# Optimization experiments

Hardware: AMD Instinct MI355X
Metric: run time of the kernel (lower is better)

The kernel has to match this reference:

```python
import jax, jax.numpy as jnp
import numpy as np

N, E, D = 50000, 800000, 128
BN_EPS = 1e-5
COORDS_WEIGHT = 1.0


def _p(key, shape, scale=0.05):
    return (jax.random.normal(key, shape, dtype=jnp.float32) * scale)


def setup_inputs() -> dict:
    key = jax.random.key(0)
    ks = jax.random.split(key, 16)
    inp = {
        "h": jax.random.normal(ks[0], (N, D), dtype=jnp.float32),
        "coord": jax.random.normal(ks[1], (N, 3), dtype=jnp.float32),
        "edge_index": jax.random.randint(ks[2], (2, E), 0, N, dtype=jnp.int32),
        # edge_mlp: Linear(2D+1 -> D), BN, ReLU, Linear(D -> D), BN, ReLU
        "e_w1": _p(ks[3], (D, 2 * D + 1)), "e_b1": jnp.zeros((D,), jnp.float32),
        "e_g1": jnp.ones((D,), jnp.float32), "e_be1": jnp.zeros((D,), jnp.float32),
        "e_w2": _p(ks[4], (D, D)), "e_b2": jnp.zeros((D,), jnp.float32),
        "e_g2": jnp.ones((D,), jnp.float32), "e_be2": jnp.zeros((D,), jnp.float32),
        # node_mlp: Linear(D + D -> D), BN, ReLU, Linear(D -> D)
        "n_w1": _p(ks[5], (D, 2 * D)), "n_b1": jnp.zeros((D,), jnp.float32),
        "n_g1": jnp.ones((D,), jnp.float32), "n_be1": jnp.zeros((D,), jnp.float32),
        "n_w2": _p(ks[6], (D, D)), "n_b2": jnp.zeros((D,), jnp.float32),
        # coord_mlp: Linear(D -> D), BN, ReLU, Linear(D -> 1, bias=False, tiny init)
        "c_w1": _p(ks[7], (D, D)), "c_b1": jnp.zeros((D,), jnp.float32),
        "c_g1": jnp.ones((D,), jnp.float32), "c_be1": jnp.zeros((D,), jnp.float32),
        "c_w2": _p(ks[8], (1, D), scale=0.001),
    }
    return inp


def _bn(x, g, b):
    # BatchNorm1d in training mode: biased batch stats over dim 0
    m = jnp.mean(x, axis=0)
    v = jnp.var(x, axis=0)
    return (x - m) * jax.lax.rsqrt(v + BN_EPS) * g + b


def _segment_mean(data, seg, num_segments):
    s = jax.ops.segment_sum(data, seg, num_segments=num_segments)
    c = jax.ops.segment_sum(jnp.ones((data.shape[0], 1), data.dtype), seg,
                            num_segments=num_segments)
    return s / jnp.maximum(c, 1.0)


def reference(h, coord, edge_index,
              e_w1, e_b1, e_g1, e_be1, e_w2, e_b2, e_g2, e_be2,
              n_w1, n_b1, n_g1, n_be1, n_w2, n_b2,
              c_w1, c_b1, c_g1, c_be1, c_w2):
    row, col = edge_index[0], edge_index[1]
    # coord2radial
    coord_diff = coord[row] - coord[col]                      # [E,3]
    radial = jnp.sum(coord_diff ** 2, axis=1, keepdims=True)  # [E,1]
    # edge_model
    e_in = jnp.concatenate([h[row], h[col], radial], axis=1)  # [E, 2D+1]
    x = jax.nn.relu(_bn(e_in @ e_w1.T + e_b1, e_g1, e_be1))
    edge_feat = jax.nn.relu(_bn(x @ e_w2.T + e_b2, e_g2, e_be2))  # [E,D]
    # coord_model
    y = jax.nn.relu(_bn(edge_feat @ c_w1.T + c_b1, c_g1, c_be1))
    scale = y @ c_w2.T                                        # [E,1]
    trans = jnp.clip(coord_diff * scale, -100.0, 100.0)
    coord_out = coord + _segment_mean(trans, row, coord.shape[0]) * COORDS_WEIGHT
    # node_model
    agg = _segment_mean(edge_feat, row, h.shape[0])           # [N,D]
    n_in = jnp.concatenate([h, agg], axis=1)                  # [N,2D]
    z = jax.nn.relu(_bn(n_in @ n_w1.T + n_b1, n_g1, n_be1))
    h_out = h + (z @ n_w2.T + n_b2)                           # recurrent residual
    return (h_out, coord_out)
```

## Files before the change

### kernel.cpp

```cpp
#include <hip/hip_runtime.h>

#define Nn 50000
#define En 800000
#define NSLOT 64

typedef __attribute__((ext_vector_type(8))) short short8;
typedef __attribute__((ext_vector_type(4))) float f32x4;

union U8 { uint4 u4; unsigned short us[8]; short8 s8; };

static __device__ __forceinline__ float bf2f(unsigned int lo16) {
  return __uint_as_float(lo16 << 16);
}
static __device__ __forceinline__ unsigned short f2bf(float f) {
  unsigned int x = __float_as_uint(f);
  return (unsigned short)((x + 0x7FFFu + ((x >> 16) & 1u)) >> 16);
}


__global__ __launch_bounds__(256) void k_prep_h(const float* __restrict__ h,
                                                unsigned short* __restrict__ nodeA) {
  int idx = blockIdx.x * 256 + threadIdx.x;
  if (idx >= Nn * 128) return;
  int n = idx >> 7, k = idx & 127;
  nodeA[(size_t)n * 256 + k] = f2bf(h[idx]);
}

__global__ __launch_bounds__(256) void k_prep_w(const float* __restrict__ src,
                                                unsigned short* __restrict__ dst, int Ksrc,
                                                int koff, int kshift, int total) {
  int idx = blockIdx.x * 256 + threadIdx.x;
  if (idx >= total) return;
  int n = idx >> kshift;
  int k = idx & ((1 << kshift) - 1);
  dst[idx] = f2bf(src[n * Ksrc + koff + k]);
}

__global__ void k_wlast(const float* __restrict__ e_w1, float* __restrict__ wlast) {
  int t = threadIdx.x;
  if (t < 128) wlast[t] = e_w1[t * 257 + 256];
}


__global__ __launch_bounds__(256) void k_count(const int* __restrict__ row, int* __restrict__ cnt) {
  int e = blockIdx.x * 256 + threadIdx.x;
  atomicAdd(&cnt[row[e]], 1);
}

__global__ __launch_bounds__(256) void k_fill(const int* __restrict__ row,
                                              const int* __restrict__ col,
                                              int* __restrict__ cursor,
                                              unsigned short* __restrict__ rowS,
                                              unsigned short* __restrict__ colS) {
  int e = blockIdx.x * 256 + threadIdx.x;
  int r = row[e];
  int pos = atomicAdd(&cursor[r], 1);
  rowS[pos] = (unsigned short)r;
  colS[pos] = (unsigned short)col[e];
}

__global__ __launch_bounds__(1024) void k_scan(const int* __restrict__ cnt, int* __restrict__ start,
                                               int* __restrict__ cursor, int n) {
  __shared__ int wsum[16];
  __shared__ int carry;
  int tid = threadIdx.x, lane = tid & 63, wid = tid >> 6;
  if (tid == 0) carry = 0;
  __syncthreads();
  for (int base = 0; base < n; base += 1024) {
    int i = base + tid;
    int v = (i < n) ? cnt[i] : 0;
    int x = v;
#pragma unroll
    for (int d = 1; d < 64; d <<= 1) {
      int y = __shfl_up(x, d, 64);
      if (lane >= d) x += y;
    }
    if (lane == 63) wsum[wid] = x;
    __syncthreads();
    if (wid == 0) {
      int s = (lane < 16) ? wsum[lane] : 0;
#pragma unroll
      for (int d = 1; d < 16; d <<= 1) {
        int y = __shfl_up(s, d, 64);
        if (lane >= d) s += y;
      }
      if (lane < 16) wsum[lane] = s;
    }
    __syncthreads();
    int c0 = carry;
    int waveoff = (wid > 0) ? wsum[wid - 1] : 0;
    int incl = c0 + waveoff + x;
    if (i < n) {
      start[i] = incl - v;
      cursor[i] = incl - v;
    }
    __syncthreads();
    if (tid == 1023) carry = incl;
    __syncthreads();
  }
}


__global__ void k_fin(const float* __restrict__ statS, const float* __restrict__ statQ,
                      const float* __restrict__ g, const float* __restrict__ be, float invR,
                      float* __restrict__ bnS, float* __restrict__ bnSh) {
  int c = threadIdx.x;
  if (c >= 128) return;
  float s = 0.f, q = 0.f;
  for (int k = 0; k < NSLOT; ++k) {
    s += statS[k * 128 + c];
    q += statQ[k * 128 + c];
  }
  float mean = s * invR;
  float var = fmaxf(q * invR - mean * mean, 0.f);
  float rs = rsqrtf(var + 1e-5f);
  float sc = g[c] * rs;
  bnS[c] = sc;
  bnSh[c] = be[c] - mean * sc;
}

template <int KSTEPS, bool BN_A, bool STATS, bool FP32OUT, bool STORE>
__global__ __launch_bounds__(256) void k_gemmW(
    const unsigned short* __restrict__ A, int Astride,
    const unsigned short* __restrict__ W, const float* __restrict__ bias,
    const float* __restrict__ bnS, const float* __restrict__ bnSh,
    unsigned short* __restrict__ outb, float* __restrict__ statS, float* __restrict__ statQ,
    const float* __restrict__ hres, float* __restrict__ outf, int R) {
  constexpr int K = KSTEPS * 32;
  constexpr int WST = K + 8;
  constexpr int SEGS = K / 8;
  __shared__ __align__(16) unsigned short smem[128 * WST];
  __shared__ float ssum[4][128], ssq[4][128];
  int tid = threadIdx.x;
  int w = tid >> 6, lane = tid & 63, m = lane & 15, kq = lane >> 4;
  int rbase = blockIdx.x * 128;
#pragma unroll
  for (int it = 0; it < SEGS / 2; ++it) {
    int idx = it * 256 + tid;
    int n = idx / SEGS, seg = idx % SEGS;
    uint4 v = *(const uint4*)(W + (size_t)n * K + seg * 8);
    *(uint4*)(smem + n * WST + seg * 8) = v;
  }
  __syncthreads();
  int row0 = rbase + w * 32 + m;
  int rc0 = min(row0, R - 1);
  int rc1 = min(row0 + 16, R - 1);
  f32x4 acc[2][8];
#pragma unroll
  for (int rt = 0; rt < 2; ++rt)
#pragma unroll
    for (int c = 0; c < 8; ++c) acc[rt][c] = (f32x4){0.f, 0.f, 0.f, 0.f};
#pragma unroll
  for (int ks = 0; ks < KSTEPS; ++ks) {
    int k0 = ks * 32 + kq * 8;
    U8 ua0, ua1;
    ua0.u4 = *(const uint4*)(A + (size_t)rc0 * Astride + k0);
    ua1.u4 = *(const uint4*)(A + (size_t)rc1 * Astride + k0);
    if (BN_A) {
      const float4* sp = (const float4*)(bnS + k0);
      const float4* hp = (const float4*)(bnSh + k0);
      float4 s0 = sp[0], s1 = sp[1], h0 = hp[0], h1 = hp[1];
      float sv[8] = {s0.x, s0.y, s0.z, s0.w, s1.x, s1.y, s1.z, s1.w};
      float hv[8] = {h0.x, h0.y, h0.z, h0.w, h1.x, h1.y, h1.z, h1.w};
#pragma unroll
      for (int j = 0; j < 8; ++j) {
        ua0.us[j] = f2bf(fmaxf(bf2f(ua0.us[j]) * sv[j] + hv[j], 0.f));
        ua1.us[j] = f2bf(fmaxf(bf2f(ua1.us[j]) * sv[j] + hv[j], 0.f));
      }
    }
#pragma unroll
    for (int c = 0; c < 8; ++c) {
      U8 ub;
      ub.u4 = *(const uint4*)(smem + (c * 16 + m) * WST + k0);
      acc[0][c] = __builtin_amdgcn_mfma_f32_16x16x32_bf16(ua0.s8, ub.s8, acc[0][c], 0, 0, 0);
      acc[1][c] = __builtin_amdgcn_mfma_f32_16x16x32_bf16(ua1.s8, ub.s8, acc[1][c], 0, 0, 0);
    }
  }
  if constexpr (FP32OUT) {
#pragma unroll
    for (int rt = 0; rt < 2; ++rt)
#pragma unroll
      for (int c = 0; c < 8; ++c) {
        int n = c * 16 + m;
        float bn_ = bias[n];
#pragma unroll
        for (int j = 0; j < 4; ++j) {
          int rr = rbase + w * 32 + rt * 16 + kq * 4 + j;
          if (rr < R) {
            size_t o = (size_t)rr * 128 + n;
            outf[o] = acc[rt][c][j] + bn_ + hres[o];
          }
        }
      }
  } else {
    if constexpr (STORE) __syncthreads();
    unsigned short* tile = smem;
#pragma unroll
    for (int c = 0; c < 8; ++c) {
      int n = c * 16 + m;
      float bn_ = bias ? bias[n] : 0.f;
      float s = 0.f, q = 0.f;
#pragma unroll
      for (int rt = 0; rt < 2; ++rt)
#pragma unroll
        for (int j = 0; j < 4; ++j) {
          int lr = w * 32 + rt * 16 + kq * 4 + j;
          float v = acc[rt][c][j] + bn_;
          if (STORE) tile[lr * 136 + n] = f2bf(v);
          if (STATS) {
            float sv = (rbase + lr < R) ? v : 0.f;
            s += sv;
            q = fmaf(sv, sv, q);
          }
        }
      if (STATS) {
        s += __shfl_xor(s, 16, 64); s += __shfl_xor(s, 32, 64);
        q += __shfl_xor(q, 16, 64); q += __shfl_xor(q, 32, 64);
        if (kq == 0) { ssum[w][n] = s; ssq[w][n] = q; }
      }
    }
    if constexpr (STORE) {
      __syncthreads();
      const uint4* tl = (const uint4*)tile;
#pragma unroll
      for (int u = 0; u < 8; ++u) {
        int idx = u * 256 + tid;
        int rr = idx >> 4, seg = idx & 15;
        if (rbase + rr < R)
          *(uint4*)(outb + (size_t)(rbase + rr) * 128 + seg * 8) = tl[rr * 17 + seg];
      }
    }
    if (STATS) {
      __syncthreads();
      if (tid < 128) {
        float s = ssum[0][tid] + ssum[1][tid] + ssum[2][tid] + ssum[3][tid];
        float q = ssq[0][tid] + ssq[1][tid] + ssq[2][tid] + ssq[3][tid];
        int slot = blockIdx.x & (NSLOT - 1);
        atomicAdd(&statS[slot * 128 + tid], s);
        atomicAdd(&statQ[slot * 128 + tid], q);
      }
    }
  }
}

__global__ __launch_bounds__(256) void k_stats1(
    const unsigned short* __restrict__ hWr, const unsigned short* __restrict__ hWc,
    const float* __restrict__ coord, const unsigned short* __restrict__ rowS,
    const unsigned short* __restrict__ colS, const float* __restrict__ wlast,
    float* __restrict__ radS, float* __restrict__ statS, float* __restrict__ statQ,
    int per_wave) {
  int tid = threadIdx.x, lane = tid & 63;
  int wid = blockIdx.x * 4 + (tid >> 6);
  int e0 = wid * per_wave;
  int e1 = min(e0 + per_wave, En);
  int c2 = lane * 2;
  float wl0 = wlast[c2], wl1 = wlast[c2 + 1];
  float s0 = 0.f, s1 = 0.f, q0 = 0.f, q1 = 0.f;
  for (int e = e0; e < e1; e += 2) {
    int ra = rowS[e], ca = colS[e];
    int rb = rowS[e + 1], cb = colS[e + 1];
    float ax = coord[ra * 3 + 0] - coord[ca * 3 + 0];
    float ay = coord[ra * 3 + 1] - coord[ca * 3 + 1];
    float az = coord[ra * 3 + 2] - coord[ca * 3 + 2];
    float bx = coord[rb * 3 + 0] - coord[cb * 3 + 0];
    float by = coord[rb * 3 + 1] - coord[cb * 3 + 1];
    float bz = coord[rb * 3 + 2] - coord[cb * 3 + 2];
    float rada = ax * ax + ay * ay + az * az;
    float radb = bx * bx + by * by + bz * bz;
    if (lane == 0) {
      radS[e] = rada;
      radS[e + 1] = radb;
    }
    unsigned int uar = *(const unsigned int*)(hWr + (size_t)ra * 128 + c2);
    unsigned int uac = *(const unsigned int*)(hWc + (size_t)ca * 128 + c2);
    unsigned int ubr = *(const unsigned int*)(hWr + (size_t)rb * 128 + c2);
    unsigned int ubc = *(const unsigned int*)(hWc + (size_t)cb * 128 + c2);
    float va0 = bf2f(uar & 0xFFFFu) + bf2f(uac & 0xFFFFu) + rada * wl0;
    float va1 = bf2f(uar >> 16) + bf2f(uac >> 16) + rada * wl1;
    float vb0 = bf2f(ubr & 0xFFFFu) + bf2f(ubc & 0xFFFFu) + radb * wl0;
    float vb1 = bf2f(ubr >> 16) + bf2f(ubc >> 16) + radb * wl1;
    s0 += va0 + vb0;
    s1 += va1 + vb1;
    q0 = fmaf(va0, va0, q0); q0 = fmaf(vb0, vb0, q0);
    q1 = fmaf(va1, va1, q1); q1 = fmaf(vb1, vb1, q1);
  }
  int slot = wid & (NSLOT - 1);
  atomicAdd(&statS[slot * 128 + c2], s0);
  atomicAdd(&statS[slot * 128 + c2 + 1], s1);
  atomicAdd(&statQ[slot * 128 + c2], q0);
  atomicAdd(&statQ[slot * 128 + c2 + 1], q1);
}

__global__ __launch_bounds__(256) void k_egemm2(
    const unsigned short* __restrict__ hWr, const unsigned short* __restrict__ hWc,
    const float* __restrict__ radS, const unsigned short* __restrict__ rowS,
    const unsigned short* __restrict__ colS, const unsigned short* __restrict__ W,
    const float* __restrict__ bias, const float* __restrict__ wlast,
    const float* __restrict__ bnS1, const float* __restrict__ bnSh1,
    unsigned short* __restrict__ outb, float* __restrict__ statS, float* __restrict__ statQ) {
  constexpr int WST = 136;
  __shared__ __align__(16) unsigned short smem[128 * WST];
  __shared__ float ssum[4][128], ssq[4][128];
  int tid = threadIdx.x;
  int w = tid >> 6, lane = tid & 63, m = lane & 15, kq = lane >> 4;
  int rbase = blockIdx.x * 128;
#pragma unroll
  for (int it = 0; it < 8; ++it) {
    int idx = it * 256 + tid;
    int n = idx >> 4, seg = idx & 15;
    uint4 v = *(const uint4*)(W + (size_t)n * 128 + seg * 8);
    *(uint4*)(smem + n * WST + seg * 8) = v;
  }
  int rc0 = rbase + w * 32 + m, rc1 = rc0 + 16;
  int r0 = rowS[rc0], c0 = colS[rc0];
  int r1 = rowS[rc1], c1 = colS[rc1];
  float rad0 = radS[rc0], rad1 = radS[rc1];
  __syncthreads();
  f32x4 acc[2][8];
#pragma unroll
  for (int rt = 0; rt < 2; ++rt)
#pragma unroll
    for (int c = 0; c < 8; ++c) acc[rt][c] = (f32x4){0.f, 0.f, 0.f, 0.f};
#pragma unroll
  for (int ks = 0; ks < 4; ++ks) {
    int k0 = ks * 32 + kq * 8;
    U8 a0r, a0c, a1r, a1c;
    a0r.u4 = *(const uint4*)(hWr + (size_t)r0 * 128 + k0);
    a0c.u4 = *(const uint4*)(hWc + (size_t)c0 * 128 + k0);
    a1r.u4 = *(const uint4*)(hWr + (size_t)r1 * 128 + k0);
    a1c.u4 = *(const uint4*)(hWc + (size_t)c1 * 128 + k0);
    const float4* wp = (const float4*)(wlast + k0);
    const float4* sp = (const float4*)(bnS1 + k0);
    const float4* hp = (const float4*)(bnSh1 + k0);
    float4 w0 = wp[0], w1 = wp[1], sA = sp[0], sB = sp[1], hA = hp[0], hB = hp[1];
    float wv[8] = {w0.x, w0.y, w0.z, w0.w, w1.x, w1.y, w1.z, w1.w};
    float sv[8] = {sA.x, sA.y, sA.z, sA.w, sB.x, sB.y, sB.z, sB.w};
    float hv[8] = {hA.x, hA.y, hA.z, hA.w, hB.x, hB.y, hB.z, hB.w};
    U8 ua0, ua1;
#pragma unroll
    for (int j = 0; j < 8; ++j) {
      float v0 = bf2f(a0r.us[j]) + bf2f(a0c.us[j]) + rad0 * wv[j];
      float v1 = bf2f(a1r.us[j]) + bf2f(a1c.us[j]) + rad1 * wv[j];
      ua0.us[j] = f2bf(fmaxf(v0 * sv[j] + hv[j], 0.f));
      ua1.us[j] = f2bf(fmaxf(v1 * sv[j] + hv[j], 0.f));
    }
#pragma unroll
    for (int c = 0; c < 8; ++c) {
      U8 ub;
      ub.u4 = *(const uint4*)(smem + (c * 16 + m) * WST + k0);
      acc[0][c] = __builtin_amdgcn_mfma_f32_16x16x32_bf16(ua0.s8, ub.s8, acc[0][c], 0, 0, 0);
      acc[1][c] = __builtin_amdgcn_mfma_f32_16x16x32_bf16(ua1.s8, ub.s8, acc[1][c], 0, 0, 0);
    }
  }
  __syncthreads();
  unsigned short* tile = smem;
#pragma unroll
  for (int c = 0; c < 8; ++c) {
    int n = c * 16 + m;
    float bn_ = bias[n];
    float s = 0.f, q = 0.f;
#pragma unroll
    for (int rt = 0; rt < 2; ++rt)
#pragma unroll
      for (int j = 0; j < 4; ++j) {
        int lr = w * 32 + rt * 16 + kq * 4 + j;
        float v = acc[rt][c][j] + bn_;
        tile[lr * 136 + n] = f2bf(v);
        s += v;
        q = fmaf(v, v, q);
      }
    s += __shfl_xor(s, 16, 64); s += __shfl_xor(s, 32, 64);
    q += __shfl_xor(q, 16, 64); q += __shfl_xor(q, 32, 64);
    if (kq == 0) { ssum[w][n] = s; ssq[w][n] = q; }
  }
  __syncthreads();
  const uint4* tl = (const uint4*)tile;
#pragma unroll
  for (int u = 0; u < 8; ++u) {
    int idx = u * 256 + tid;
    int rr = idx >> 4, seg = idx & 15;
    *(uint4*)(outb + (size_t)(rbase + rr) * 128 + seg * 8) = tl[rr * 17 + seg];
  }
  if (tid < 128) {
    float s = ssum[0][tid] + ssum[1][tid] + ssum[2][tid] + ssum[3][tid];
    float q = ssq[0][tid] + ssq[1][tid] + ssq[2][tid] + ssq[3][tid];
    int slot = blockIdx.x & (NSLOT - 1);
    atomicAdd(&statS[slot * 128 + tid], s);
    atomicAdd(&statQ[slot * 128 + tid], q);
  }
}

__global__ __launch_bounds__(256) void k_agg(const unsigned short* __restrict__ t,
                                             const int* __restrict__ start,
                                             const int* __restrict__ cnt,
                                             const float* __restrict__ bnS,
                                             const float* __restrict__ bnSh,
                                             unsigned short* __restrict__ nodeA) {
  int tid = threadIdx.x;
  int lane = tid & 63;
  int n = blockIdx.x * 4 + (tid >> 6);
  if (n >= Nn) return;
  int deg = cnt[n], off = start[n];
  int c2 = lane * 2;
  float s0 = bnS[c2], s1 = bnS[c2 + 1], h0 = bnSh[c2], h1 = bnSh[c2 + 1];
  float a0 = 0.f, a1 = 0.f;
  const unsigned short* p = t + (size_t)off * 128 + c2;
  for (int j = 0; j < deg; ++j) {
    unsigned int u = *(const unsigned int*)(p + (size_t)j * 128);
    a0 += fmaxf(bf2f(u & 0xFFFFu) * s0 + h0, 0.f);
    a1 += fmaxf(bf2f(u >> 16) * s1 + h1, 0.f);
  }
  float inv = 1.f / fmaxf((float)deg, 1.f);
  unsigned int o = (unsigned)f2bf(a0 * inv) | ((unsigned)f2bf(a1 * inv) << 16);
  *(unsigned int*)(nodeA + (size_t)n * 256 + 128 + c2) = o;
}

__global__ __launch_bounds__(256) void k_scale2(const unsigned short* __restrict__ t,
                                                const float* __restrict__ bnS3,
                                                const float* __restrict__ bnSh3,
                                                const float* __restrict__ cw2,
                                                float* __restrict__ scaleE) {
  int tid = threadIdx.x, lane = tid & 63, w = tid >> 6;
  long e = (long)blockIdx.x * 8 + w * 2;
  int c2 = lane * 2;
  float s0 = bnS3[c2], s1 = bnS3[c2 + 1];
  float h0 = bnSh3[c2], h1 = bnSh3[c2 + 1];
  float w0 = cw2[c2], w1 = cw2[c2 + 1];
  unsigned int ua = *(const unsigned int*)(t + e * 128 + c2);
  unsigned int ub = *(const unsigned int*)(t + (e + 1) * 128 + c2);
  float pa = fmaxf(bf2f(ua & 0xFFFFu) * s0 + h0, 0.f) * w0 +
             fmaxf(bf2f(ua >> 16) * s1 + h1, 0.f) * w1;
  float pb = fmaxf(bf2f(ub & 0xFFFFu) * s0 + h0, 0.f) * w0 +
             fmaxf(bf2f(ub >> 16) * s1 + h1, 0.f) * w1;
#pragma unroll
  for (int d = 32; d; d >>= 1) {
    pa += __shfl_xor(pa, d, 64);
    pb += __shfl_xor(pb, d, 64);
  }
  if (lane == 0) {
    scaleE[e] = pa;
    scaleE[e + 1] = pb;
  }
}

__global__ __launch_bounds__(256) void k_coord(const float* __restrict__ coord,
                                               const unsigned short* __restrict__ colS,
                                               const int* __restrict__ start,
                                               const int* __restrict__ cnt,
                                               const float* __restrict__ scaleE,
                                               float* __restrict__ cout) {
  int tid = threadIdx.x;
  int lane = tid & 63;
  int n = blockIdx.x * 4 + (tid >> 6);
  if (n >= Nn) return;
  int deg = cnt[n], off = start[n];
  float cx0 = coord[n * 3 + 0], cy0 = coord[n * 3 + 1], cz0 = coord[n * 3 + 2];
  float ax = 0.f, ay = 0.f, az = 0.f;
  for (int j = lane; j < deg; j += 64) {
    int e = off + j;
    int c = colS[e];
    float s = scaleE[e];
    float tx = (cx0 - coord[c * 3 + 0]) * s;
    float ty = (cy0 - coord[c * 3 + 1]) * s;
    float tz = (cz0 - coord[c * 3 + 2]) * s;
    ax += fminf(fmaxf(tx, -100.f), 100.f);
    ay += fminf(fmaxf(ty, -100.f), 100.f);
    az += fminf(fmaxf(tz, -100.f), 100.f);
  }
#pragma unroll
  for (int d = 32; d; d >>= 1) {
    ax += __shfl_xor(ax, d, 64);
    ay += __shfl_xor(ay, d, 64);
    az += __shfl_xor(az, d, 64);
  }
  if (lane == 0) {
    float inv = 1.f / fmaxf((float)deg, 1.f);
    cout[n * 3 + 0] = cx0 + ax * inv;
    cout[n * 3 + 1] = cy0 + ay * inv;
    cout[n * 3 + 2] = cz0 + az * inv;
  }
}


extern "C" void kernel_launch(void* const* d_in, const int* in_sizes, int n_in, void* d_out,
                              int out_size, void* d_ws, size_t ws_size, hipStream_t stream) {
  (void)in_sizes; (void)n_in; (void)out_size; (void)ws_size;
  const float* h = (const float*)d_in[0];
  const float* coord = (const float*)d_in[1];
  const int* eidx = (const int*)d_in[2];
  const int* row = eidx;
  const int* col = eidx + En;
  const float* e_w1 = (const float*)d_in[3];
  const float* e_b1 = (const float*)d_in[4];
  const float* e_g1 = (const float*)d_in[5];
  const float* e_be1 = (const float*)d_in[6];
  const float* e_w2 = (const float*)d_in[7];
  const float* e_b2 = (const float*)d_in[8];
  const float* e_g2 = (const float*)d_in[9];
  const float* e_be2 = (const float*)d_in[10];
  const float* n_w1 = (const float*)d_in[11];
  const float* n_b1 = (const float*)d_in[12];
  const float* n_g1 = (const float*)d_in[13];
  const float* n_be1 = (const float*)d_in[14];
  const float* n_w2 = (const float*)d_in[15];
  const float* n_b2 = (const float*)d_in[16];
  const float* c_w1 = (const float*)d_in[17];
  const float* c_b1 = (const float*)d_in[18];
  const float* c_g1 = (const float*)d_in[19];
  const float* c_be1 = (const float*)d_in[20];
  const float* c_w2 = (const float*)d_in[21];

  char* base = (char*)d_ws;
  size_t off = 0;
  auto alloc = [&](size_t bytes) -> void* {
    void* p = base + off;
    off = (off + bytes + 255) & ~(size_t)255;
    return p;
  };
  unsigned short* t = (unsigned short*)alloc((size_t)En * 128 * 2);
  unsigned short* nodeA = (unsigned short*)alloc((size_t)Nn * 256 * 2);
  unsigned short* hWr = (unsigned short*)alloc((size_t)Nn * 128 * 2);
  unsigned short* hWc = (unsigned short*)alloc((size_t)Nn * 128 * 2);
  float* scaleE = (float*)alloc((size_t)En * 4);
  float* radS = scaleE;
  unsigned short* rowS = (unsigned short*)alloc((size_t)En * 2);
  unsigned short* colS = (unsigned short*)alloc((size_t)En * 2);
  int* cnt = (int*)alloc((size_t)Nn * 4);
  int* startp = (int*)alloc((size_t)Nn * 4);
  int* cursor = (int*)alloc((size_t)Nn * 4);
  float* statS = (float*)alloc(4 * NSLOT * 128 * 4);
  float* statQ = (float*)alloc(4 * NSLOT * 128 * 4);
  float* bnS = (float*)alloc(4 * 128 * 4);
  float* bnSh = (float*)alloc(4 * 128 * 4);
  unsigned short* w1a = (unsigned short*)alloc(128 * 128 * 2);
  unsigned short* w1b = (unsigned short*)alloc(128 * 128 * 2);
  unsigned short* w2b = (unsigned short*)alloc(128 * 128 * 2);
  unsigned short* c1b = (unsigned short*)alloc(128 * 128 * 2);
  unsigned short* n1b = (unsigned short*)alloc(128 * 256 * 2);
  unsigned short* n2b = (unsigned short*)alloc(128 * 128 * 2);
  float* wlast = (float*)alloc(128 * 4);

  hipMemsetAsync(cnt, 0, (size_t)Nn * 4, stream);
  hipMemsetAsync(statS, 0, 4 * NSLOT * 128 * 4, stream);
  hipMemsetAsync(statQ, 0, 4 * NSLOT * 128 * 4, stream);

  k_prep_h<<<(Nn * 128 + 255) / 256, 256, 0, stream>>>(h, nodeA);
  k_prep_w<<<(128 * 128 + 255) / 256, 256, 0, stream>>>(e_w1, w1a, 257, 0, 7, 128 * 128);
  k_prep_w<<<(128 * 128 + 255) / 256, 256, 0, stream>>>(e_w1, w1b, 257, 128, 7, 128 * 128);
  k_prep_w<<<(128 * 128 + 255) / 256, 256, 0, stream>>>(e_w2, w2b, 128, 0, 7, 128 * 128);
  k_prep_w<<<(128 * 128 + 255) / 256, 256, 0, stream>>>(c_w1, c1b, 128, 0, 7, 128 * 128);
  k_prep_w<<<(128 * 256 + 255) / 256, 256, 0, stream>>>(n_w1, n1b, 256, 0, 8, 128 * 256);
  k_prep_w<<<(128 * 128 + 255) / 256, 256, 0, stream>>>(n_w2, n2b, 128, 0, 7, 128 * 128);
  k_wlast<<<1, 128, 0, stream>>>(e_w1, wlast);

  k_count<<<En / 256, 256, 0, stream>>>(row, cnt);
  k_scan<<<1, 1024, 0, stream>>>(cnt, startp, cursor, Nn);
  k_fill<<<En / 256, 256, 0, stream>>>(row, col, cursor, rowS, colS);

  const int gridN = (Nn + 127) / 128;
  k_gemmW<4, false, false, false, true><<<gridN, 256, 0, stream>>>(
      nodeA, 256, w1a, e_b1, nullptr, nullptr, hWr, nullptr, nullptr, nullptr, nullptr, Nn);
  k_gemmW<4, false, false, false, true><<<gridN, 256, 0, stream>>>(
      nodeA, 256, w1b, nullptr, nullptr, nullptr, hWc, nullptr, nullptr, nullptr, nullptr, Nn);

  const int per_wave = ((En / 2 + 5119) / 5120) * 2;
  k_stats1<<<1280, 256, 0, stream>>>(hWr, hWc, coord, rowS, colS, wlast, radS,
                                     statS + 0 * NSLOT * 128, statQ + 0 * NSLOT * 128, per_wave);
  k_fin<<<1, 128, 0, stream>>>(statS + 0 * NSLOT * 128, statQ + 0 * NSLOT * 128, e_g1, e_be1,
                               1.f / En, bnS + 0, bnSh + 0);

  k_egemm2<<<En / 128, 256, 0, stream>>>(hWr, hWc, radS, rowS, colS, w2b, e_b2, wlast, bnS + 0,
                                         bnSh + 0, t, statS + 1 * NSLOT * 128,
                                         statQ + 1 * NSLOT * 128);
  k_fin<<<1, 128, 0, stream>>>(statS + 1 * NSLOT * 128, statQ + 1 * NSLOT * 128, e_g2, e_be2,
                               1.f / En, bnS + 128, bnSh + 128);

  k_agg<<<(Nn + 3) / 4, 256, 0, stream>>>(t, startp, cnt, bnS + 128, bnSh + 128, nodeA);

  k_gemmW<4, true, true, false, true><<<En / 128, 256, 0, stream>>>(
      t, 128, c1b, c_b1, bnS + 128, bnSh + 128, t, statS + 2 * NSLOT * 128,
      statQ + 2 * NSLOT * 128, nullptr, nullptr, En);
  k_fin<<<1, 128, 0, stream>>>(statS + 2 * NSLOT * 128, statQ + 2 * NSLOT * 128, c_g1, c_be1,
                               1.f / En, bnS + 256, bnSh + 256);

  k_scale2<<<En / 8, 256, 0, stream>>>(t, bnS + 256, bnSh + 256, c_w2, scaleE);

  float* hout = (float*)d_out;
  float* cout = hout + (size_t)Nn * 128;
  k_coord<<<(Nn + 3) / 4, 256, 0, stream>>>(coord, colS, startp, cnt, scaleE, cout);

  k_gemmW<8, false, true, false, true><<<gridN, 256, 0, stream>>>(
      nodeA, 256, n1b, n_b1, nullptr, nullptr, t, statS + 3 * NSLOT * 128,
      statQ + 3 * NSLOT * 128, nullptr, nullptr, Nn);
  k_fin<<<1, 128, 0, stream>>>(statS + 3 * NSLOT * 128, statQ + 3 * NSLOT * 128, n_g1, n_be1,
                               1.f / Nn, bnS + 384, bnSh + 384);
  k_gemmW<4, true, false, true, true><<<gridN, 256, 0, stream>>>(
      t, 128, n2b, n_b2, bnS + 384, bnSh + 384, nullptr, nullptr, nullptr, h, hout, Nn);
}
```

Measured before the change: 787.5 us.

## Compute coord-MLP BN stats from second moments and fuse scale projection into GEMM

The coord MLP's first-layer BatchNorm statistics are now derived algebraically from the Gram matrix Y^T Y and the column sums of the activated edge features (k_moment, k_msum, k_fin3). This removes the need to materialise the coord GEMM output before its stats are known. A second GEMM pass (k_cgemm) then applies BN, ReLU and the final projection in registers and writes only the per-edge scale, replacing the write and re-read of the E×128 intermediate and the separate k_scale2 kernel. It also adds packed bf16 conversion via v_cvt_pk_bf16_f32, at the cost of an extra 128×128 MFMA pass over all edges, a partial-matrix reduction, and a variance formula that can lose precision through cancellation.

After: 917.7 us. 1.17x slower.

```diff
diff --git a/kernel.cpp b/kernel.cpp
--- a/kernel.cpp
+++ b/kernel.cpp
@@ -3,11 +3,12 @@
 #define Nn 50000
 #define En 800000
 #define NSLOT 64
+#define MGRID 384
 
 typedef __attribute__((ext_vector_type(8))) short short8;
 typedef __attribute__((ext_vector_type(4))) float f32x4;
 
-union U8 { uint4 u4; unsigned short us[8]; short8 s8; };
+union U8 { uint4 u4; unsigned short us[8]; unsigned int ui[4]; short8 s8; };
 
 static __device__ __forceinline__ float bf2f(unsigned int lo16) {
   return __uint_as_float(lo16 << 16);
@@ -15,6 +16,11 @@
 static __device__ __forceinline__ unsigned short f2bf(float f) {
   unsigned int x = __float_as_uint(f);
   return (unsigned short)((x + 0x7FFFu + ((x >> 16) & 1u)) >> 16);
+}
+static __device__ __forceinline__ unsigned int f2bf2(float a, float b) {
+  unsigned int r;
+  asm("v_cvt_pk_bf16_f32 %0, %1, %2" : "=v"(r) : "v"(a), "v"(b));
+  return r;
 }
 
 
@@ -162,11 +168,18 @@
       float4 s0 = sp[0], s1 = sp[1], h0 = hp[0], h1 = hp[1];
       float sv[8] = {s0.x, s0.y, s0.z, s0.w, s1.x, s1.y, s1.z, s1.w};
       float hv[8] = {h0.x, h0.y, h0.z, h0.w, h1.x, h1.y, h1.z, h1.w};
-#pragma unroll
-      for (int j = 0; j < 8; ++j) {
-        ua0.us[j] = f2bf(fmaxf(bf2f(ua0.us[j]) * sv[j] + hv[j], 0.f));
-        ua1.us[j] = f2bf(fmaxf(bf2f(ua1.us[j]) * sv[j] + hv[j], 0.f));
+      U8 pa, pb;
+#pragma unroll
+      for (int jj = 0; jj < 4; ++jj) {
+        float a0 = fmaxf(bf2f(ua0.us[2 * jj]) * sv[2 * jj] + hv[2 * jj], 0.f);
+        float a1 = fmaxf(bf2f(ua0.us[2 * jj + 1]) * sv[2 * jj + 1] + hv[2 * jj + 1], 0.f);
+        float b0 = fmaxf(bf2f(ua1.us[2 * jj]) * sv[2 * jj] + hv[2 * jj], 0.f);
+        float b1 = fmaxf(bf2f(ua1.us[2 * jj + 1]) * sv[2 * jj + 1] + hv[2 * jj + 1], 0.f);
+        pa.ui[jj] = f2bf2(a0, a1);
+        pb.ui[jj] = f2bf2(b0, b1);
       }
+      ua0 = pa;
+      ua1 = pb;
     }
 #pragma unroll
     for (int c = 0; c < 8; ++c) {
@@ -338,11 +351,18 @@
     float hv[8] = {hA.x, hA.y, hA.z, hA.w, hB.x, hB.y, hB.z, hB.w};
     U8 ua0, ua1;
 #pragma unroll
-    for (int j = 0; j < 8; ++j) {
-      float v0 = bf2f(a0r.us[j]) + bf2f(a0c.us[j]) + rad0 * wv[j];
-      float v1 = bf2f(a1r.us[j]) + bf2f(a1c.us[j]) + rad1 * wv[j];
-      ua0.us[j] = f2bf(fmaxf(v0 * sv[j] + hv[j], 0.f));
-      ua1.us[j] = f2bf(fmaxf(v1 * sv[j] + hv[j], 0.f));
+    for (int jj = 0; jj < 4; ++jj) {
+      int j0 = 2 * jj, j1 = 2 * jj + 1;
+      float v0a = bf2f(a0r.us[j0]) + bf2f(a0c.us[j0]) + rad0 * wv[j0];
+      float v0b = bf2f(a0r.us[j1]) + bf2f(a0c.us[j1]) + rad0 * wv[j1];
+      float v1a = bf2f(a1r.us[j0]) + bf2f(a1c.us[j0]) + rad1 * wv[j0];
+      float v1b = bf2f(a1r.us[j1]) + bf2f(a1c.us[j1]) + rad1 * wv[j1];
+      v0a = fmaxf(v0a * sv[j0] + hv[j0], 0.f);
+      v0b = fmaxf(v0b * sv[j1] + hv[j1], 0.f);
+      v1a = fmaxf(v1a * sv[j0] + hv[j0], 0.f);
+      v1b = fmaxf(v1b * sv[j1] + hv[j1], 0.f);
+      ua0.ui[jj] = f2bf2(v0a, v0b);
+      ua1.ui[jj] = f2bf2(v1a, v1b);
     }
 #pragma unroll
     for (int c = 0; c < 8; ++c) {
@@ -415,31 +435,209 @@
   *(unsigned int*)(nodeA + (size_t)n * 256 + 128 + c2) = o;
 }
 
-__global__ __launch_bounds__(256) void k_scale2(const unsigned short* __restrict__ t,
-                                                const float* __restrict__ bnS3,
-                                                const float* __restrict__ bnSh3,
-                                                const float* __restrict__ cw2,
-                                                float* __restrict__ scaleE) {
-  int tid = threadIdx.x, lane = tid & 63, w = tid >> 6;
-  long e = (long)blockIdx.x * 8 + w * 2;
-  int c2 = lane * 2;
-  float s0 = bnS3[c2], s1 = bnS3[c2 + 1];
-  float h0 = bnSh3[c2], h1 = bnSh3[c2 + 1];
-  float w0 = cw2[c2], w1 = cw2[c2 + 1];
-  unsigned int ua = *(const unsigned int*)(t + e * 128 + c2);
-  unsigned int ub = *(const unsigned int*)(t + (e + 1) * 128 + c2);
-  float pa = fmaxf(bf2f(ua & 0xFFFFu) * s0 + h0, 0.f) * w0 +
-             fmaxf(bf2f(ua >> 16) * s1 + h1, 0.f) * w1;
-  float pb = fmaxf(bf2f(ub & 0xFFFFu) * s0 + h0, 0.f) * w0 +
-             fmaxf(bf2f(ub >> 16) * s1 + h1, 0.f) * w1;
-#pragma unroll
-  for (int d = 32; d; d >>= 1) {
-    pa += __shfl_xor(pa, d, 64);
-    pb += __shfl_xor(pb, d, 64);
-  }
-  if (lane == 0) {
-    scaleE[e] = pa;
-    scaleE[e + 1] = pb;
+__global__ __launch_bounds__(256) void k_moment(
+    const unsigned short* __restrict__ t,
+    const float* __restrict__ bnS2, const float* __restrict__ bnSh2,
+    float* __restrict__ Mpart, float* __restrict__ SyG) {
+  constexpr int WST = 136;
+  __shared__ __align__(16) unsigned short yT[128 * WST];
+  __shared__ float s2L[128], h2L[128];
+  int tid = threadIdx.x;
+  int w = tid >> 6, lane = tid & 63, m = lane & 15, kq = lane >> 4;
+  if (tid < 128) { s2L[tid] = bnS2[tid]; h2L[tid] = bnSh2[tid]; }
+  f32x4 acc[2][8];
+#pragma unroll
+  for (int rt = 0; rt < 2; ++rt)
+#pragma unroll
+    for (int c = 0; c < 8; ++c) acc[rt][c] = (f32x4){0.f, 0.f, 0.f, 0.f};
+  float sy[32];
+#pragma unroll
+  for (int i = 0; i < 32; ++i) sy[i] = 0.f;
+  for (int tile = blockIdx.x; tile < En / 128; tile += MGRID) {
+    __syncthreads();
+    int e0 = tile * 128 + lane * 2;
+    U8 ra[4], rb[4];
+#pragma unroll
+    for (int q = 0; q < 4; ++q) {
+      ra[q].u4 = *(const uint4*)(t + (size_t)e0 * 128 + w * 32 + q * 8);
+      rb[q].u4 = *(const uint4*)(t + (size_t)(e0 + 1) * 128 + w * 32 + q * 8);
+    }
+#pragma unroll
+    for (int q = 0; q < 4; ++q)
+#pragma unroll
+      for (int i = 0; i < 8; ++i) {
+        int c = w * 32 + q * 8 + i;
+        float s = s2L[c], h = h2L[c];
+        float ya = fmaxf(bf2f(ra[q].us[i]) * s + h, 0.f);
+        float yb = fmaxf(bf2f(rb[q].us[i]) * s + h, 0.f);
+        sy[q * 8 + i] += ya + yb;
+        *(unsigned int*)(yT + c * WST + lane * 2) = f2bf2(ya, yb);
+      }
+    __syncthreads();
+#pragma unroll
+    for (int ks = 0; ks < 4; ++ks) {
+      int k0 = ks * 32 + kq * 8;
+      U8 a0, a1;
+      a0.u4 = *(const uint4*)(yT + (w * 32 + m) * WST + k0);
+      a1.u4 = *(const uint4*)(yT + (w * 32 + 16 + m) * WST + k0);
+#pragma unroll
+      for (int c = 0; c < 8; ++c) {
+        U8 ub;
+        ub.u4 = *(const uint4*)(yT + (c * 16 + m) * WST + k0);
+        acc[0][c] = __builtin_amdgcn_mfma_f32_16x16x32_bf16(a0.s8, ub.s8, acc[0][c], 0, 0, 0);
+        acc[1][c] = __builtin_amdgcn_mfma_f32_16x16x32_bf16(a1.s8, ub.s8, acc[1][c], 0, 0, 0);
+      }
+    }
+  }
+  size_t mb = (size_t)blockIdx.x * 16384;
+#pragma unroll
+  for (int rt = 0; rt < 2; ++rt)
+#pragma unroll
+    for (int c = 0; c < 8; ++c)
+#pragma unroll
+      for (int j = 0; j < 4; ++j)
+        Mpart[mb + (size_t)(w * 32 + rt * 16 + kq * 4 + j) * 128 + c * 16 + m] = acc[rt][c][j];
+#pragma unroll
+  for (int i = 0; i < 32; ++i) {
+    float s = sy[i];
+#pragma unroll
+    for (int d = 1; d < 64; d <<= 1) s += __shfl_xor(s, d, 64);
+    if (lane == 0) atomicAdd(&SyG[w * 32 + i], s);
+  }
+}
+
+__global__ __launch_bounds__(256) void k_msum(const float* __restrict__ Mpart,
+                                              float* __restrict__ Mg) {
+  __shared__ float red[4][64];
+  int tid = threadIdx.x;
+  int e = blockIdx.x * 64 + (tid & 63);
+  int pq = tid >> 6;
+  float s = 0.f;
+  for (int k = pq * (MGRID / 4); k < (pq + 1) * (MGRID / 4); ++k)
+    s += Mpart[(size_t)k * 16384 + e];
+  red[pq][tid & 63] = s;
+  __syncthreads();
+  if (tid < 64) Mg[e] = red[0][tid] + red[1][tid] + red[2][tid] + red[3][tid];
+}
+
+__global__ __launch_bounds__(128) void k_fin3(
+    const float* __restrict__ Mg, const float* __restrict__ Sy,
+    const float* __restrict__ w1, const float* __restrict__ g,
+    const float* __restrict__ be, float invE,
+    float* __restrict__ bnS3, float* __restrict__ bnSh3) {
+  __shared__ float sW[128];
+  __shared__ float r2[4];
+  int c = blockIdx.x, j = threadIdx.x;
+  sW[j] = w1[c * 128 + j];
+  __syncthreads();
+  float a0 = 0.f, a1 = 0.f, a2 = 0.f, a3 = 0.f;
+  for (int i = 0; i < 128; i += 4) {
+    a0 = fmaf(sW[i], Mg[i * 128 + j], a0);
+    a1 = fmaf(sW[i + 1], Mg[(i + 1) * 128 + j], a1);
+    a2 = fmaf(sW[i + 2], Mg[(i + 2) * 128 + j], a2);
+    a3 = fmaf(sW[i + 3], Mg[(i + 3) * 128 + j], a3);
+  }
+  float q = sW[j] * ((a0 + a1) + (a2 + a3));
+  float dm = sW[j] * Sy[j];
+#pragma unroll
+  for (int d = 1; d < 64; d <<= 1) {
+    q += __shfl_xor(q, d, 64);
+    dm += __shfl_xor(dm, d, 64);
+  }
+  int wv = j >> 6;
+  if ((j & 63) == 0) { r2[wv * 2] = q; r2[wv * 2 + 1] = dm; }
+  __syncthreads();
+  if (j == 0) {
+    float quad = r2[0] + r2[2];
+    float dmt = r2[1] + r2[3];
+    float Eu = dmt * invE;
+    float var = fmaxf(quad * invE - Eu * Eu, 0.f);
+    float S = g[c] * rsqrtf(var + 1e-5f);
+    bnS3[c] = S;
+    bnSh3[c] = be[c] - Eu * S;
+  }
+}
+
+__global__ __launch_bounds__(256) void k_cgemm(
+    const unsigned short* __restrict__ A,
+    const unsigned short* __restrict__ W,
+    const float* __restrict__ bnS2, const float* __restrict__ bnSh2,
+    const float* __restrict__ bnS3, const float* __restrict__ bnSh3,
+    const float* __restrict__ cw2, float* __restrict__ scaleE) {
+  constexpr int WST = 136;
+  __shared__ __align__(16) unsigned short smem[128 * WST];
+  int tid = threadIdx.x;
+  int w = tid >> 6, lane = tid & 63, m = lane & 15, kq = lane >> 4;
+  int rbase = blockIdx.x * 128;
+#pragma unroll
+  for (int it = 0; it < 8; ++it) {
+    int idx = it * 256 + tid;
+    int n = idx >> 4, seg = idx & 15;
+    *(uint4*)(smem + n * WST + seg * 8) = *(const uint4*)(W + (size_t)n * 128 + seg * 8);
+  }
+  __syncthreads();
+  int rc0 = rbase + w * 32 + m, rc1 = rc0 + 16;
+  f32x4 acc[2][8];
+#pragma unroll
+  for (int rt = 0; rt < 2; ++rt)
+#pragma unroll
+    for (int c = 0; c < 8; ++c) acc[rt][c] = (f32x4){0.f, 0.f, 0.f, 0.f};
+#pragma unroll
+  for (int ks = 0; ks < 4; ++ks) {
+    int k0 = ks * 32 + kq * 8;
+    U8 ua0, ua1;
+    ua0.u4 = *(const uint4*)(A + (size_t)rc0 * 128 + k0);
+    ua1.u4 = *(const uint4*)(A + (size_t)rc1 * 128 + k0);
+    const float4* sp = (const float4*)(bnS2 + k0);
+    const float4* hp = (const float4*)(bnSh2 + k0);
+    float4 s0 = sp[0], s1 = sp[1], h0 = hp[0], h1 = hp[1];
+    float sv[8] = {s0.x, s0.y, s0.z, s0.w, s1.x, s1.y, s1.z, s1.w};
+    float hv[8] = {h0.x, h0.y, h0.z, h0.w, h1.x, h1.y, h1.z, h1.w};
+    U8 pa, pb;
+#pragma unroll
+    for (int jj = 0; jj < 4; ++jj) {
+      float v0a = fmaxf(bf2f(ua0.us[2 * jj]) * sv[2 * jj] + hv[2 * jj], 0.f);
+      float v0b = fmaxf(bf2f(ua0.us[2 * jj + 1]) * sv[2 * jj + 1] + hv[2 * jj + 1], 0.f);
+      float v1a = fmaxf(bf2f(ua1.us[2 * jj]) * sv[2 * jj] + hv[2 * jj], 0.f);
+      float v1b = fmaxf(bf2f(ua1.us[2 * jj + 1]) * sv[2 * jj + 1] + hv[2 * jj + 1], 0.f);
+      pa.ui[jj] = f2bf2(v0a, v0b);
+      pb.ui[jj] = f2bf2(v1a, v1b);
+    }
+#pragma unroll
+    for (int c = 0; c < 8; ++c) {
+      U8 ub;
+      ub.u4 = *(const uint4*)(smem + (c * 16 + m) * WST + k0);
+      acc[0][c] = __builtin_amdgcn_mfma_f32_16x16x32_bf16(pa.s8, ub.s8, acc[0][c], 0, 0, 0);
+      acc[1][c] = __builtin_amdgcn_mfma_f32_16x16x32_bf16(pb.s8, ub.s8, acc[1][c], 0, 0, 0);
+    }
+  }
+  float s3v[8], h3v[8], wv[8];
+#pragma unroll
+  for (int c = 0; c < 8; ++c) {
+    int n = c * 16 + m;
+    s3v[c] = bnS3[n];
+    h3v[c] = bnSh3[n];
+    wv[c] = cw2[n];
+  }
+  float p0[4] = {0.f, 0.f, 0.f, 0.f}, p1[4] = {0.f, 0.f, 0.f, 0.f};
+#pragma unroll
+  for (int c = 0; c < 8; ++c)
+#pragma unroll
+    for (int j = 0; j < 4; ++j) {
+      p0[j] += fmaxf(acc[0][c][j] * s3v[c] + h3v[c], 0.f) * wv[c];
+      p1[j] += fmaxf(acc[1][c][j] * s3v[c] + h3v[c], 0.f) * wv[c];
+    }
+#pragma unroll
+  for (int j = 0; j < 4; ++j)
+#pragma unroll
+    for (int d = 1; d < 16; d <<= 1) {
+      p0[j] += __shfl_xor(p0[j], d, 64);
+      p1[j] += __shfl_xor(p1[j], d, 64);
+    }
+  if (m == 0) {
+    int r0 = rbase + w * 32 + kq * 4;
+    *(float4*)(scaleE + r0) = make_float4(p0[0], p0[1], p0[2], p0[3]);
+    *(float4*)(scaleE + r0 + 16) = make_float4(p1[0], p1[1], p1[2], p1[3]);
   }
 }
 
@@ -506,6 +704,7 @@
   const float* n_b2 = (const float*)d_in[16];
   const float* c_w1 = (const float*)d_in[17];
   const float* c_b1 = (const float*)d_in[18];
+  (void)c_b1;
   const float* c_g1 = (const float*)d_in[19];
   const float* c_be1 = (const float*)d_in[20];
   const float* c_w2 = (const float*)d_in[21];
@@ -539,6 +738,9 @@
   unsigned short* n1b = (unsigned short*)alloc(128 * 256 * 2);
   unsigned short* n2b = (unsigned short*)alloc(128 * 128 * 2);
   float* wlast = (float*)alloc(128 * 4);
+  float* Mpart = (float*)hWr;
+  float* Mg = scaleE;
+  float* SyG = scaleE + 16384;
 
   hipMemsetAsync(cnt, 0, (size_t)Nn * 4, stream);
   hipMemsetAsync(statS, 0, 4 * NSLOT * 128 * 4, stream);
@@ -577,13 +779,13 @@
 
   k_agg<<<(Nn + 3) / 4, 256, 0, stream>>>(t, startp, cnt, bnS + 128, bnSh + 128, nodeA);
 
-  k_gemmW<4, true, true, false, true><<<En / 128, 256, 0, stream>>>(
-      t, 128, c1b, c_b1, bnS + 128, bnSh + 128, t, statS + 2 * NSLOT * 128,
-      statQ + 2 * NSLOT * 128, nullptr, nullptr, En);
-  k_fin<<<1, 128, 0, stream>>>(statS + 2 * NSLOT * 128, statQ + 2 * NSLOT * 128, c_g1, c_be1,
-                               1.f / En, bnS + 256, bnSh + 256);
-
-  k_scale2<<<En / 8, 256, 0, stream>>>(t, bnS + 256, bnSh + 256, c_w2, scaleE);
+  hipMemsetAsync(SyG, 0, 128 * 4, stream);
+  k_moment<<<MGRID, 256, 0, stream>>>(t, bnS + 128, bnSh + 128, Mpart, SyG);
+  k_msum<<<256, 256, 0, stream>>>(Mpart, Mg);
+  k_fin3<<<128, 128, 0, stream>>>(Mg, SyG, c_w1, c_g1, c_be1, 1.f / En, bnS + 256, bnSh + 256);
+
+  k_cgemm<<<En / 128, 256, 0, stream>>>(t, c1b, bnS + 128, bnSh + 128, bnS + 256, bnSh + 256,
+                                        c_w2, scaleE);
 
   float* hout = (float*)d_out;
   float* cout = hout + (size_t)Nn * 128;
```
